# Kernel tuning notes

Hardware: AMD Instinct MI355X
Metric: run time of the kernel (lower is better)

## Reference

```python
import jax, jax.numpy as jnp
import numpy as np

NUM_HEADS = 8

def setup_inputs() -> dict:
    key = jax.random.key(0)
    k1, k2, k3 = jax.random.split(key, 3)
    B, N, C = 4, 4096, 512
    x = jax.random.normal(k1, (B, N, C), dtype=jnp.float32)
    w_qkv = jax.random.normal(k2, (C, 3 * C), dtype=jnp.float32) * (1.0 / np.sqrt(C))
    w_proj = jax.random.normal(k3, (C, C), dtype=jnp.float32) * (1.0 / np.sqrt(C))
    b_proj = jnp.zeros((C,), dtype=jnp.float32)
    return {"x": x, "w_qkv": w_qkv, "w_proj": w_proj, "b_proj": b_proj}

def reference(x, w_qkv, w_proj, b_proj):
    B, N, C = x.shape
    H = NUM_HEADS
    D = C // H
    # qkv projection (no bias), split into q, k, v of shape [B, H, N, D]
    qkv = (x @ w_qkv).reshape(B, N, 3, H, D)
    qkv = jnp.transpose(qkv, (2, 0, 3, 1, 4))
    q, k, v = qkv[0], qkv[1], qkv[2]
    # q: softmax over head_dim; k: elu(k)+1 then softmax over sequence dim
    q = jax.nn.softmax(q, axis=-1)
    k = jax.nn.softmax(jax.nn.elu(k) + 1.0, axis=-2)
    # linear attention: context = k^T @ v  -> [B, H, D, D]
    context = jnp.einsum('bhnd,bhne->bhde', k, v)
    # out = q @ context -> [B, H, N, D]
    out = jnp.einsum('bhnd,bhde->bhne', q, context)
    out = jnp.transpose(out, (0, 2, 1, 3)).reshape(B, N, C)
    # output projection (dropout with p=0.0 is identity)
    return out @ w_proj + b_proj
```

## Files before the change

### kernel.cpp

```cpp
#include <hip/hip_runtime.h>
#include <hip/hip_bf16.h>

typedef unsigned short u16;
typedef __attribute__((ext_vector_type(8))) short bhalf8;
typedef __attribute__((ext_vector_type(4))) float fx4;

struct __align__(8) US4 { u16 v[4]; };

__device__ __forceinline__ u16 f2bf(float x) {
  union { float f; unsigned int u; } c; c.f = x;
  unsigned int r = c.u + 0x7FFFu + ((c.u >> 16) & 1u);
  return (u16)(r >> 16);
}

__device__ __forceinline__ float bf2f(u16 v) {
  union { unsigned int u; float f; } c; c.u = ((unsigned int)v) << 16;
  return c.f;
}

__device__ __forceinline__ void gload16(const void* g, void* l) {
  __builtin_amdgcn_global_load_lds((const __attribute__((address_space(1))) void*)g,
                                   (__attribute__((address_space(3))) void*)l,
                                   16, 0, 0);
}

#define MFMA16(a, b, c) __builtin_amdgcn_mfma_f32_16x16x32_bf16((a), (b), (c), 0, 0, 0)

__global__ __launch_bounds__(256)
void k_prep(const float* __restrict__ x, u16* __restrict__ xb,
            const float* __restrict__ wqkv, u16* __restrict__ wqT,
            const float* __restrict__ wproj, u16* __restrict__ wpT) {
  __shared__ float tile[64][65];
  const int bx = blockIdx.x;
  const int t = threadIdx.x;
  if (bx < 8192) {
    int i = bx * 256 + t;
    float4 v = ((const float4*)x)[i];
    US4 o;
    o.v[0] = f2bf(v.x); o.v[1] = f2bf(v.y); o.v[2] = f2bf(v.z); o.v[3] = f2bf(v.w);
    ((US4*)xb)[i] = o;
    return;
  }
  const float* in; u16* out; int C, remap, bx2;
  if (bx < 8384) { in = wqkv; out = wqT; C = 1536; remap = 1; bx2 = bx - 8192; }
  else           { in = wproj; out = wpT; C = 512;  remap = 0; bx2 = bx - 8384; }
  const int rt = bx2 & 7, ct = bx2 >> 3;
  const int r0 = rt * 64, c0 = ct * 64;
  #pragma unroll
  for (int i = 0; i < 16; ++i) {
    int e = i * 256 + t;
    int rr = e >> 6, cc = e & 63;
    tile[rr][cc] = in[(r0 + rr) * C + c0 + cc];
  }
  __syncthreads();
  #pragma unroll
  for (int i = 0; i < 16; ++i) {
    int e = i * 256 + t;
    int rr = e >> 6, cc = e & 63;
    int orow = c0 + rr;
    if (remap && orow >= 512) {
      int region = (orow - 512) >> 9;
      int within = (orow - 512) & 511;
      int h = within >> 6;
      orow = 512 + h * 128 + region * 64 + (within & 63);
    }
    out[orow * 512 + r0 + cc] = f2bf(tile[cc][rr]);
  }
}

__device__ __forceinline__ void gemm_core512(const char* Ab, const char* Bb,
                                             char* As, char* Bs, fx4 acc[4][4]) {
  const int t = threadIdx.x;
  const int w = t >> 6, l = t & 63;
  const int wm = w >> 2, wn = w & 3;
  #pragma unroll 1
  for (int kt = 0; kt < 8; ++kt) {
    __syncthreads();
    const int kb = kt * 128;
    #pragma unroll
    for (int i = 0; i < 2; ++i) {
      int off = (i * 512 + t) * 16;
      int row = off >> 7;
      int scol = (off & 127) ^ ((row & 7) << 4);
      gload16(Ab + row * 1024 + kb + scol, As + off);
    }
    #pragma unroll
    for (int i = 0; i < 4; ++i) {
      int off = (i * 512 + t) * 16;
      int row = off >> 7;
      int scol = (off & 127) ^ ((row & 7) << 4);
      gload16(Bb + row * 1024 + kb + scol, Bs + off);
    }
    asm volatile("s_waitcnt vmcnt(0)" ::: "memory");
    __syncthreads();
    #pragma unroll
    for (int ks = 0; ks < 2; ++ks) {
      bhalf8 af[4], bfv[4];
      const int kbyte = ks * 64 + ((l >> 4) * 16);
      #pragma unroll
      for (int f = 0; f < 4; ++f) {
        int ra = wm * 64 + f * 16 + (l & 15);
        af[f] = *(const bhalf8*)(As + ra * 128 + (kbyte ^ ((ra & 7) << 4)));
        int rb = wn * 64 + f * 16 + (l & 15);
        bfv[f] = *(const bhalf8*)(Bs + rb * 128 + (kbyte ^ ((rb & 7) << 4)));
      }
      #pragma unroll
      for (int fm = 0; fm < 4; ++fm)
        #pragma unroll
        for (int fn = 0; fn < 4; ++fn)
          acc[fm][fn] = MFMA16(af[fm], bfv[fn], acc[fm][fn]);
    }
  }
}

__device__ __forceinline__ void gemm_core256(const char* Ab, const char* Bb,
                                             char* As, char* Bs, fx4 acc[4][4]) {
  const int t = threadIdx.x;
  const int w = t >> 6, l = t & 63;
  const int wm = w >> 1, wn = w & 1;
  #pragma unroll 1
  for (int kt = 0; kt < 8; ++kt) {
    __syncthreads();
    const int kb = kt * 128;
    #pragma unroll
    for (int j = 0; j < 4; ++j) {
      int off = ((j * 4 + w) * 64 + l) * 16;
      int row = off >> 7;
      int scol = (off & 127) ^ ((row & 7) << 4);
      gload16(Ab + row * 1024 + kb + scol, As + off);
      gload16(Bb + row * 1024 + kb + scol, Bs + off);
    }
    asm volatile("s_waitcnt vmcnt(0)" ::: "memory");
    __syncthreads();
    #pragma unroll
    for (int ks = 0; ks < 2; ++ks) {
      bhalf8 af[4], bfv[4];
      const int kbyte = ks * 64 + ((l >> 4) * 16);
      #pragma unroll
      for (int f = 0; f < 4; ++f) {
        int ra = wm * 64 + f * 16 + (l & 15);
        af[f] = *(const bhalf8*)(As + ra * 128 + (kbyte ^ ((ra & 7) << 4)));
        int rb = wn * 64 + f * 16 + (l & 15);
        bfv[f] = *(const bhalf8*)(Bs + rb * 128 + (kbyte ^ ((rb & 7) << 4)));
      }
      #pragma unroll
      for (int fm = 0; fm < 4; ++fm)
        #pragma unroll
        for (int fn = 0; fn < 4; ++fn)
          acc[fm][fn] = MFMA16(af[fm], bfv[fn], acc[fm][fn]);
    }
  }
}

__global__ __launch_bounds__(512, 4)
void k_qkv_gemm(const char* __restrict__ xb, const char* __restrict__ wqT,
                u16* __restrict__ qhat, u16* __restrict__ ctx_part,
                float* __restrict__ z_part) {
  __shared__ __align__(16) char lds[65536];
  const int bx = blockIdx.x;
  const int tM = bx & 127, tN = bx >> 7;
  fx4 acc[4][4];
  const fx4 z4 = {0.f, 0.f, 0.f, 0.f};
  #pragma unroll
  for (int i = 0; i < 4; ++i)
    #pragma unroll
    for (int j = 0; j < 4; ++j) acc[i][j] = z4;

  gemm_core512(xb + tM * 131072, wqT + tN * 262144, lds, lds + 16384, acc);

  const int t = threadIdx.x, w = t >> 6, l = t & 63;
  const int wm = w >> 2, wn = w & 3;
  const int m0 = tM * 128 + wm * 64;
  const int c0 = tN * 256 + wn * 64;

  if (tN < 2) {
    #pragma unroll
    for (int fm = 0; fm < 4; ++fm) {
      #pragma unroll
      for (int fn = 0; fn < 4; ++fn)
        #pragma unroll
        for (int r = 0; r < 4; ++r)
          acc[fm][fn][r] = __expf(acc[fm][fn][r]);
      fx4 s = acc[fm][0] + acc[fm][1] + acc[fm][2] + acc[fm][3];
      fx4 inv;
      #pragma unroll
      for (int r = 0; r < 4; ++r) {
        float sv = s[r];
        sv += __shfl_xor(sv, 1, 64);
        sv += __shfl_xor(sv, 2, 64);
        sv += __shfl_xor(sv, 4, 64);
        sv += __shfl_xor(sv, 8, 64);
        inv[r] = 1.0f / sv;
      }
      #pragma unroll
      for (int fn = 0; fn < 4; ++fn)
        #pragma unroll
        for (int r = 0; r < 4; ++r) {
          int m = m0 + fm * 16 + ((l >> 4) * 4) + r;
          int c = c0 + fn * 16 + (l & 15);
          qhat[m * 512 + c] = f2bf(acc[fm][fn][r] * inv[r]);
        }
    }
  } else {
    const int hpair = tN - 2;
    const int b = tM >> 5;
    const int mt = tM & 31;
    const int hl = wn >> 1;
    const bool isK = ((wn & 1) == 0);
    char* ktb = lds + hl * 32768;
    char* vtb = ktb + 16384;
    char* dstb = isK ? ktb : vtb;
    __syncthreads();
    #pragma unroll
    for (int fm = 0; fm < 4; ++fm)
      #pragma unroll
      for (int fn = 0; fn < 4; ++fn) {
        int d = fn * 16 + (l & 15);
        int n0 = wm * 64 + fm * 16 + ((l >> 4) * 4);
        US4 p;
        #pragma unroll
        for (int r = 0; r < 4; ++r) {
          float v = acc[fm][fn][r];
          if (isK) { float tt = v > 0.f ? v + 1.f : __expf(v); v = __expf(tt); }
          p.v[r] = f2bf(v);
        }
        *(US4*)(dstb + d * 256 + ((2 * n0) ^ ((d & 7) << 4))) = p;
      }
    __syncthreads();
    const int hl2 = w >> 2;
    const int bh = b * 8 + hpair * 2 + hl2;
    char* kb2 = lds + hl2 * 32768;
    char* vb2 = kb2 + 16384;
    const int d0 = (w & 3) * 16;
    fx4 cacc[4]; fx4 zacc = z4;
    #pragma unroll
    for (int fe = 0; fe < 4; ++fe) cacc[fe] = z4;
    bhalf8 ones;
    #pragma unroll
    for (int i = 0; i < 8; ++i) ones[i] = (short)0x3F80;
    #pragma unroll
    for (int kk = 0; kk < 4; ++kk) {
      int nbyte = kk * 64 + ((l >> 4) * 16);
      int d = d0 + (l & 15);
      bhalf8 a = *(const bhalf8*)(kb2 + d * 256 + (nbyte ^ ((d & 7) << 4)));
      #pragma unroll
      for (int fe = 0; fe < 4; ++fe) {
        int e = fe * 16 + (l & 15);
        bhalf8 bv = *(const bhalf8*)(vb2 + e * 256 + (nbyte ^ ((e & 7) << 4)));
        cacc[fe] = MFMA16(a, bv, cacc[fe]);
      }
      zacc = MFMA16(a, ones, zacc);
    }
    u16* cp = ctx_part + (bh * 32 + mt) * 4096;
    #pragma unroll
    for (int fe = 0; fe < 4; ++fe)
      #pragma unroll
      for (int r = 0; r < 4; ++r) {
        int d = d0 + ((l >> 4) * 4) + r;
        int e = fe * 16 + (l & 15);
        cp[d * 64 + e] = f2bf(cacc[fe][r]);
      }
    if ((l & 15) == 0) {
      #pragma unroll
      for (int r = 0; r < 4; ++r)
        z_part[(bh * 32 + mt) * 64 + d0 + ((l >> 4) * 4) + r] = zacc[r];
    }
  }
}

__global__ __launch_bounds__(256)
void k_reduce(const u16* __restrict__ ctx_part, float* __restrict__ ctx32) {
  const int bid = blockIdx.x;
  const int bh = bid >> 2;
  const int idx0 = (bid & 3) * 1024 + threadIdx.x * 4;
  float s0 = 0.f, s1 = 0.f, s2 = 0.f, s3 = 0.f;
  #pragma unroll
  for (int mt = 0; mt < 32; ++mt) {
    US4 p = *(const US4*)(ctx_part + (bh * 32 + mt) * 4096 + idx0);
    s0 += bf2f(p.v[0]); s1 += bf2f(p.v[1]); s2 += bf2f(p.v[2]); s3 += bf2f(p.v[3]);
  }
  float4 o; o.x = s0; o.y = s1; o.z = s2; o.w = s3;
  *(float4*)(ctx32 + bh * 4096 + idx0) = o;
}

__global__ __launch_bounds__(256, 1)
void k_w2(const float* __restrict__ ctx32, const float* __restrict__ z_part,
          const u16* __restrict__ wpT, u16* __restrict__ W2T) {
  const int bh = blockIdx.x;
  const int b = bh >> 3, h = bh & 7;
  __shared__ float zinv[64];
  __shared__ __align__(16) u16 alds[64][72];
  const int t = threadIdx.x;
  if (t < 64) {
    float zs = 0.f;
    #pragma unroll
    for (int mt = 0; mt < 32; ++mt) zs += z_part[(bh * 32 + mt) * 64 + t];
    zinv[t] = 1.0f / zs;
  }
  __syncthreads();
  #pragma unroll
  for (int i = 0; i < 16; ++i) {
    int idx = i * 256 + t;
    int d = idx >> 6, e = idx & 63;
    alds[d][e] = f2bf(ctx32[bh * 4096 + idx] * zinv[d]);
  }
  __syncthreads();
  const int w = t >> 6, l = t & 63;
  fx4 acc[4][8];
  const fx4 z4 = {0.f, 0.f, 0.f, 0.f};
  #pragma unroll
  for (int i = 0; i < 4; ++i)
    #pragma unroll
    for (int j = 0; j < 8; ++j) acc[i][j] = z4;
  #pragma unroll
  for (int ks = 0; ks < 2; ++ks) {
    bhalf8 af[4];
    #pragma unroll
    for (int fm = 0; fm < 4; ++fm) {
      int row = fm * 16 + (l & 15);
      af[fm] = *(const bhalf8*)((const char*)alds + row * 144 + ks * 64 + ((l >> 4) * 16));
    }
    #pragma unroll
    for (int fn = 0; fn < 8; ++fn) {
      int c = w * 128 + fn * 16 + (l & 15);
      bhalf8 bv = *(const bhalf8*)(wpT + c * 512 + h * 64 + ks * 32 + ((l >> 4) * 8));
      #pragma unroll
      for (int fm = 0; fm < 4; ++fm)
        acc[fm][fn] = MFMA16(af[fm], bv, acc[fm][fn]);
    }
  }
  #pragma unroll
  for (int fm = 0; fm < 4; ++fm)
    #pragma unroll
    for (int fn = 0; fn < 8; ++fn) {
      int c = w * 128 + fn * 16 + (l & 15);
      int d0 = fm * 16 + ((l >> 4) * 4);
      US4 p;
      #pragma unroll
      for (int r = 0; r < 4; ++r) p.v[r] = f2bf(acc[fm][fn][r]);
      *(US4*)(W2T + (b * 512 + c) * 512 + h * 64 + d0) = p;
    }
}

__global__ __launch_bounds__(256, 2)
void k_out_gemm(const char* __restrict__ qhat, const char* __restrict__ W2T,
                const float* __restrict__ bproj, float* __restrict__ outp) {
  __shared__ __align__(16) char lds[32768];
  const int bx = blockIdx.x;
  const int tM = bx & 127, tN = bx >> 7;
  const int b = tM >> 5;
  fx4 acc[4][4];
  const fx4 z4 = {0.f, 0.f, 0.f, 0.f};
  #pragma unroll
  for (int i = 0; i < 4; ++i)
    #pragma unroll
    for (int j = 0; j < 4; ++j) acc[i][j] = z4;

  gemm_core256(qhat + tM * 131072, W2T + b * 524288 + tN * 131072, lds, lds + 16384, acc);

  const int t = threadIdx.x, w = t >> 6, l = t & 63;
  const int wm = w >> 1, wn = w & 1;
  const int m0 = tM * 128 + wm * 64;
  const int c0 = tN * 128 + wn * 64;
  #pragma unroll
  for (int fm = 0; fm < 4; ++fm)
    #pragma unroll
    for (int fn = 0; fn < 4; ++fn) {
      int c = c0 + fn * 16 + (l & 15);
      float bp = bproj[c];
      #pragma unroll
      for (int r = 0; r < 4; ++r) {
        int m = m0 + fm * 16 + ((l >> 4) * 4) + r;
        outp[m * 512 + c] = acc[fm][fn][r] + bp;
      }
    }
}

extern "C" void kernel_launch(void* const* d_in, const int* in_sizes, int n_in,
                              void* d_out, int out_size, void* d_ws, size_t ws_size,
                              hipStream_t stream) {
  (void)in_sizes; (void)n_in; (void)out_size;
  const float* x     = (const float*)d_in[0];
  const float* wqkv  = (const float*)d_in[1];
  const float* wproj = (const float*)d_in[2];
  const float* bproj = (const float*)d_in[3];
  float* outp = (float*)d_out;
  char* ws = (char*)d_ws;

  char* xb   = ws;
  char* wqT  = ws + 16777216;
  char* wpT  = ws + 18350080;
  char* qhat = ws + 18874368;
  char* ctxp = ws + 35651584;
  char* zp   = ws + 44040192;
  char* ctx32= ws + 44302336;
  char* w2t  = ws + 44826624;
  if (ws_size < 46923776) return;

  k_prep<<<8448, 256, 0, stream>>>(x, (u16*)xb, wqkv, (u16*)wqT, wproj, (u16*)wpT);
  k_qkv_gemm<<<768, 512, 0, stream>>>(xb, wqT, (u16*)qhat, (u16*)ctxp, (float*)zp);
  k_reduce<<<128, 256, 0, stream>>>((const u16*)ctxp, (float*)ctx32);
  k_w2<<<32, 256, 0, stream>>>((const float*)ctx32, (const float*)zp, (const u16*)wpT, (u16*)w2t);
  k_out_gemm<<<512, 256, 0, stream>>>(qhat, w2t, bproj, outp);
}
```

Measured before the change: 80.43 us.

## Enlarge QKV GEMM tile to 256x256 with double-buffered ping-pong LDS pipeline

The QKV GEMM tile grows from 128x256 to 256x256, halving the grid to 384 blocks. The main loop now double-buffers LDS (128 KB), stages the next k-tile in quarters between MFMA quadrants, and uses s_setprio and split barriers to overlap global loads with matrix math. The partial context and normaliser counts drop from 32 to 16 per head, which shrinks the reduce work and the workspace. In exchange, more registers and LDS are used per block, which lowers occupancy, and the tail wave is coarser with fewer blocks.

```diff
diff --git a/kernel.cpp b/kernel.cpp
--- a/kernel.cpp
+++ b/kernel.cpp
@@ -68,120 +68,146 @@
   }
 }
 
-__device__ __forceinline__ void gemm_core512(const char* Ab, const char* Bb,
-                                             char* As, char* Bs, fx4 acc[4][4]) {
-  const int t = threadIdx.x;
-  const int w = t >> 6, l = t & 63;
-  const int wm = w >> 2, wn = w & 3;
-  #pragma unroll 1
-  for (int kt = 0; kt < 8; ++kt) {
-    __syncthreads();
-    const int kb = kt * 128;
-    #pragma unroll
-    for (int i = 0; i < 2; ++i) {
-      int off = (i * 512 + t) * 16;
-      int row = off >> 7;
-      int scol = (off & 127) ^ ((row & 7) << 4);
-      gload16(Ab + row * 1024 + kb + scol, As + off);
-    }
-    #pragma unroll
-    for (int i = 0; i < 4; ++i) {
-      int off = (i * 512 + t) * 16;
-      int row = off >> 7;
-      int scol = (off & 127) ^ ((row & 7) << 4);
-      gload16(Bb + row * 1024 + kb + scol, Bs + off);
-    }
-    asm volatile("s_waitcnt vmcnt(0)" ::: "memory");
-    __syncthreads();
-    #pragma unroll
-    for (int ks = 0; ks < 2; ++ks) {
-      bhalf8 af[4], bfv[4];
-      const int kbyte = ks * 64 + ((l >> 4) * 16);
-      #pragma unroll
-      for (int f = 0; f < 4; ++f) {
-        int ra = wm * 64 + f * 16 + (l & 15);
-        af[f] = *(const bhalf8*)(As + ra * 128 + (kbyte ^ ((ra & 7) << 4)));
-        int rb = wn * 64 + f * 16 + (l & 15);
-        bfv[f] = *(const bhalf8*)(Bs + rb * 128 + (kbyte ^ ((rb & 7) << 4)));
-      }
-      #pragma unroll
-      for (int fm = 0; fm < 4; ++fm)
-        #pragma unroll
-        for (int fn = 0; fn < 4; ++fn)
-          acc[fm][fn] = MFMA16(af[fm], bfv[fn], acc[fm][fn]);
-    }
-  }
-}
-
-__device__ __forceinline__ void gemm_core256(const char* Ab, const char* Bb,
-                                             char* As, char* Bs, fx4 acc[4][4]) {
-  const int t = threadIdx.x;
-  const int w = t >> 6, l = t & 63;
-  const int wm = w >> 1, wn = w & 1;
-  #pragma unroll 1
-  for (int kt = 0; kt < 8; ++kt) {
-    __syncthreads();
-    const int kb = kt * 128;
-    #pragma unroll
-    for (int j = 0; j < 4; ++j) {
-      int off = ((j * 4 + w) * 64 + l) * 16;
-      int row = off >> 7;
-      int scol = (off & 127) ^ ((row & 7) << 4);
-      gload16(Ab + row * 1024 + kb + scol, As + off);
-      gload16(Bb + row * 1024 + kb + scol, Bs + off);
-    }
-    asm volatile("s_waitcnt vmcnt(0)" ::: "memory");
-    __syncthreads();
-    #pragma unroll
-    for (int ks = 0; ks < 2; ++ks) {
-      bhalf8 af[4], bfv[4];
-      const int kbyte = ks * 64 + ((l >> 4) * 16);
-      #pragma unroll
-      for (int f = 0; f < 4; ++f) {
-        int ra = wm * 64 + f * 16 + (l & 15);
-        af[f] = *(const bhalf8*)(As + ra * 128 + (kbyte ^ ((ra & 7) << 4)));
-        int rb = wn * 64 + f * 16 + (l & 15);
-        bfv[f] = *(const bhalf8*)(Bs + rb * 128 + (kbyte ^ ((rb & 7) << 4)));
-      }
-      #pragma unroll
-      for (int fm = 0; fm < 4; ++fm)
-        #pragma unroll
-        for (int fn = 0; fn < 4; ++fn)
-          acc[fm][fn] = MFMA16(af[fm], bfv[fn], acc[fm][fn]);
-    }
-  }
-}
-
-__global__ __launch_bounds__(512, 4)
+__device__ __forceinline__ void stage_half_A(const char* Ab, char* buf, int kt, int hf, int t) {
+  #pragma unroll
+  for (int j = 0; j < 2; ++j) {
+    int o = (j * 512 + t) * 16;
+    int r = o >> 7;
+    int m = (r & 63) | ((r >> 6) << 7) | (hf << 6);
+    gload16(Ab + m * 1024 + kt * 128 + ((o & 127) ^ ((r & 7) << 4)),
+            buf + hf * 16384 + o);
+  }
+}
+__device__ __forceinline__ void stage_half_B(const char* Bb, char* buf, int kt, int hf, int t) {
+  #pragma unroll
+  for (int j = 0; j < 2; ++j) {
+    int o = (j * 512 + t) * 16;
+    int r = o >> 7;
+    int c = (r & 31) | ((r >> 5) << 6) | (hf << 5);
+    gload16(Bb + c * 1024 + kt * 128 + ((o & 127) ^ ((r & 7) << 4)),
+            buf + 32768 + hf * 16384 + o);
+  }
+}
+
+__global__ __launch_bounds__(512, 2)
 void k_qkv_gemm(const char* __restrict__ xb, const char* __restrict__ wqT,
                 u16* __restrict__ qhat, u16* __restrict__ ctx_part,
                 float* __restrict__ z_part) {
-  __shared__ __align__(16) char lds[65536];
+  __shared__ __align__(16) char lds[131072];
   const int bx = blockIdx.x;
-  const int tM = bx & 127, tN = bx >> 7;
-  fx4 acc[4][4];
+  const int tM = bx & 63, tN = bx >> 6;
+  const char* Ab = xb + tM * 262144;
+  const char* Bb = wqT + tN * 262144;
+  const int tid = threadIdx.x;
+  const int w = tid >> 6, l = tid & 63;
+  const int wm = w >> 2, wn = w & 3;
+
+  fx4 acc[8][4];
   const fx4 z4 = {0.f, 0.f, 0.f, 0.f};
   #pragma unroll
-  for (int i = 0; i < 4; ++i)
+  for (int i = 0; i < 8; ++i)
     #pragma unroll
     for (int j = 0; j < 4; ++j) acc[i][j] = z4;
 
-  gemm_core512(xb + tM * 131072, wqT + tN * 262144, lds, lds + 16384, acc);
-
-  const int t = threadIdx.x, w = t >> 6, l = t & 63;
-  const int wm = w >> 2, wn = w & 3;
-  const int m0 = tM * 128 + wm * 64;
-  const int c0 = tN * 256 + wn * 64;
+  bhalf8 a[8], b0[4], b1[4];
+
+#define LOAD_A(As, mq) do {                                              \
+    _Pragma("unroll") for (int ks = 0; ks < 2; ++ks) {                   \
+      const int kb_ = ks * 64 + ((l >> 4) * 16);                         \
+      _Pragma("unroll") for (int fm = 0; fm < 4; ++fm) {                 \
+        int ra_ = wm * 64 + fm * 16 + (l & 15);                          \
+        a[ks * 4 + fm] = *(const bhalf8*)((As) + (mq) * 16384 +          \
+                         ra_ * 128 + (kb_ ^ ((ra_ & 7) << 4)));          \
+      } } } while (0)
+#define LOAD_B(Bs, nq, br) do {                                          \
+    _Pragma("unroll") for (int ks = 0; ks < 2; ++ks) {                   \
+      const int kb_ = ks * 64 + ((l >> 4) * 16);                         \
+      _Pragma("unroll") for (int fn = 0; fn < 2; ++fn) {                 \
+        int rb_ = wn * 32 + fn * 16 + (l & 15);                          \
+        br[ks * 2 + fn] = *(const bhalf8*)((Bs) + 32768 + (nq) * 16384 + \
+                          rb_ * 128 + (kb_ ^ ((rb_ & 7) << 4)));         \
+      } } } while (0)
+#define MFMA_QUAD(mq, nq, br) do {                                       \
+    __builtin_amdgcn_s_setprio(1);                                       \
+    _Pragma("unroll") for (int ks = 0; ks < 2; ++ks)                     \
+      _Pragma("unroll") for (int fm = 0; fm < 4; ++fm)                   \
+        _Pragma("unroll") for (int fn = 0; fn < 2; ++fn)                 \
+          acc[(mq) * 4 + fm][(nq) * 2 + fn] =                            \
+            MFMA16(a[ks * 4 + fm], br[ks * 2 + fn],                      \
+                   acc[(mq) * 4 + fm][(nq) * 2 + fn]);                   \
+    __builtin_amdgcn_s_setprio(0);                                       \
+  } while (0)
+#define BARX()  do { __builtin_amdgcn_s_barrier();                       \
+    __builtin_amdgcn_sched_barrier(0); } while (0)
+#define LGKM0() do { asm volatile("s_waitcnt lgkmcnt(0)" ::: "memory");  \
+    __builtin_amdgcn_sched_barrier(0); } while (0)
+#define VM(N)   asm volatile("s_waitcnt vmcnt(" #N ")" ::: "memory")
+
+  stage_half_A(Ab, lds, 0, 0, tid);
+  stage_half_B(Bb, lds, 0, 0, tid);
+  stage_half_B(Bb, lds, 0, 1, tid);
+  stage_half_A(Ab, lds, 0, 1, tid);
+  VM(4);
+  BARX();
+
+  #pragma unroll 1
+  for (int kt = 0; kt < 7; ++kt) {
+    const char* As = lds + (kt & 1) * 65536;
+    char* nbuf = lds + ((kt + 1) & 1) * 65536;
+    LOAD_A(As, 0); LOAD_B(As, 0, b0);
+    stage_half_A(Ab, nbuf, kt + 1, 0, tid);
+    __builtin_amdgcn_s_barrier(); LGKM0();
+    MFMA_QUAD(0, 0, b0);
+    VM(4); BARX();
+    LOAD_B(As, 1, b1);
+    stage_half_B(Bb, nbuf, kt + 1, 0, tid);
+    __builtin_amdgcn_s_barrier(); LGKM0();
+    MFMA_QUAD(0, 1, b1);
+    VM(4); BARX();
+    LOAD_A(As, 1);
+    stage_half_B(Bb, nbuf, kt + 1, 1, tid);
+    __builtin_amdgcn_s_barrier(); LGKM0();
+    MFMA_QUAD(1, 1, b1);
+    BARX();
+    stage_half_A(Ab, nbuf, kt + 1, 1, tid);
+    __builtin_amdgcn_s_barrier();
+    MFMA_QUAD(1, 0, b0);
+    VM(4); BARX();
+  }
+  {
+    const char* As = lds + 65536;
+    LOAD_A(As, 0); LOAD_B(As, 0, b0);
+    __builtin_amdgcn_s_barrier(); LGKM0();
+    MFMA_QUAD(0, 0, b0);
+    VM(2); BARX();
+    LOAD_B(As, 1, b1);
+    __builtin_amdgcn_s_barrier(); LGKM0();
+    MFMA_QUAD(0, 1, b1);
+    VM(0); BARX();
+    LOAD_A(As, 1);
+    __builtin_amdgcn_s_barrier(); LGKM0();
+    MFMA_QUAD(1, 1, b1);
+    BARX();
+    MFMA_QUAD(1, 0, b0);
+  }
+#undef LOAD_A
+#undef LOAD_B
+#undef MFMA_QUAD
+#undef BARX
+#undef LGKM0
+#undef VM
 
   if (tN < 2) {
-    #pragma unroll
-    for (int fm = 0; fm < 4; ++fm) {
-      #pragma unroll
-      for (int fn = 0; fn < 4; ++fn)
+    const int m0 = tM * 256 + wm * 128;
+    const int c0 = tN * 256 + wn * 64;
+    #pragma unroll
+    for (int i = 0; i < 8; ++i) {
+      #pragma unroll
+      for (int j = 0; j < 4; ++j)
         #pragma unroll
         for (int r = 0; r < 4; ++r)
-          acc[fm][fn][r] = __expf(acc[fm][fn][r]);
-      fx4 s = acc[fm][0] + acc[fm][1] + acc[fm][2] + acc[fm][3];
+          acc[i][j][r] = __expf(acc[i][j][r]);
+      fx4 s = acc[i][0] + acc[i][1] + acc[i][2] + acc[i][3];
       fx4 inv;
       #pragma unroll
       for (int r = 0; r < 4; ++r) {
@@ -193,44 +219,43 @@
         inv[r] = 1.0f / sv;
       }
       #pragma unroll
-      for (int fn = 0; fn < 4; ++fn)
+      for (int j = 0; j < 4; ++j)
         #pragma unroll
         for (int r = 0; r < 4; ++r) {
-          int m = m0 + fm * 16 + ((l >> 4) * 4) + r;
-          int c = c0 + fn * 16 + (l & 15);
-          qhat[m * 512 + c] = f2bf(acc[fm][fn][r] * inv[r]);
+          int m = m0 + i * 16 + ((l >> 4) * 4) + r;
+          int c = c0 + j * 16 + (l & 15);
+          qhat[m * 512 + c] = f2bf(acc[i][j][r] * inv[r]);
         }
     }
   } else {
     const int hpair = tN - 2;
-    const int b = tM >> 5;
-    const int mt = tM & 31;
+    const int b = tM >> 4, mt = tM & 15;
     const int hl = wn >> 1;
     const bool isK = ((wn & 1) == 0);
-    char* ktb = lds + hl * 32768;
-    char* vtb = ktb + 16384;
-    char* dstb = isK ? ktb : vtb;
     __syncthreads();
-    #pragma unroll
-    for (int fm = 0; fm < 4; ++fm)
-      #pragma unroll
-      for (int fn = 0; fn < 4; ++fn) {
-        int d = fn * 16 + (l & 15);
-        int n0 = wm * 64 + fm * 16 + ((l >> 4) * 4);
+    char* kbuf = lds + hl * 65536;
+    char* vbuf = kbuf + 32768;
+    char* dstb = isK ? kbuf : vbuf;
+    #pragma unroll
+    for (int i = 0; i < 8; ++i)
+      #pragma unroll
+      for (int j = 0; j < 4; ++j) {
+        int d = j * 16 + (l & 15);
+        int n0 = wm * 128 + i * 16 + ((l >> 4) * 4);
         US4 p;
         #pragma unroll
         for (int r = 0; r < 4; ++r) {
-          float v = acc[fm][fn][r];
+          float v = acc[i][j][r];
           if (isK) { float tt = v > 0.f ? v + 1.f : __expf(v); v = __expf(tt); }
           p.v[r] = f2bf(v);
         }
-        *(US4*)(dstb + d * 256 + ((2 * n0) ^ ((d & 7) << 4))) = p;
+        *(US4*)(dstb + d * 512 + ((2 * n0) ^ ((d & 7) << 4))) = p;
       }
     __syncthreads();
     const int hl2 = w >> 2;
     const int bh = b * 8 + hpair * 2 + hl2;
-    char* kb2 = lds + hl2 * 32768;
-    char* vb2 = kb2 + 16384;
+    char* kb2 = lds + hl2 * 65536;
+    char* vb2 = kb2 + 32768;
     const int d0 = (w & 3) * 16;
     fx4 cacc[4]; fx4 zacc = z4;
     #pragma unroll
@@ -239,19 +264,19 @@
     #pragma unroll
     for (int i = 0; i < 8; ++i) ones[i] = (short)0x3F80;
     #pragma unroll
-    for (int kk = 0; kk < 4; ++kk) {
+    for (int kk = 0; kk < 8; ++kk) {
       int nbyte = kk * 64 + ((l >> 4) * 16);
       int d = d0 + (l & 15);
-      bhalf8 a = *(const bhalf8*)(kb2 + d * 256 + (nbyte ^ ((d & 7) << 4)));
+      bhalf8 av = *(const bhalf8*)(kb2 + d * 512 + (nbyte ^ ((d & 7) << 4)));
       #pragma unroll
       for (int fe = 0; fe < 4; ++fe) {
         int e = fe * 16 + (l & 15);
-        bhalf8 bv = *(const bhalf8*)(vb2 + e * 256 + (nbyte ^ ((e & 7) << 4)));
-        cacc[fe] = MFMA16(a, bv, cacc[fe]);
-      }
-      zacc = MFMA16(a, ones, zacc);
-    }
-    u16* cp = ctx_part + (bh * 32 + mt) * 4096;
+        bhalf8 bv = *(const bhalf8*)(vb2 + e * 512 + (nbyte ^ ((e & 7) << 4)));
+        cacc[fe] = MFMA16(av, bv, cacc[fe]);
+      }
+      zacc = MFMA16(av, ones, zacc);
+    }
+    u16* cp = ctx_part + (bh * 16 + mt) * 4096;
     #pragma unroll
     for (int fe = 0; fe < 4; ++fe)
       #pragma unroll
@@ -263,7 +288,7 @@
     if ((l & 15) == 0) {
       #pragma unroll
       for (int r = 0; r < 4; ++r)
-        z_part[(bh * 32 + mt) * 64 + d0 + ((l >> 4) * 4) + r] = zacc[r];
+        z_part[(bh * 16 + mt) * 64 + d0 + ((l >> 4) * 4) + r] = zacc[r];
     }
   }
 }
@@ -275,8 +300,8 @@
   const int idx0 = (bid & 3) * 1024 + threadIdx.x * 4;
   float s0 = 0.f, s1 = 0.f, s2 = 0.f, s3 = 0.f;
   #pragma unroll
-  for (int mt = 0; mt < 32; ++mt) {
-    US4 p = *(const US4*)(ctx_part + (bh * 32 + mt) * 4096 + idx0);
+  for (int mt = 0; mt < 16; ++mt) {
+    US4 p = *(const US4*)(ctx_part + (bh * 16 + mt) * 4096 + idx0);
     s0 += bf2f(p.v[0]); s1 += bf2f(p.v[1]); s2 += bf2f(p.v[2]); s3 += bf2f(p.v[3]);
   }
   float4 o; o.x = s0; o.y = s1; o.z = s2; o.w = s3;
@@ -294,7 +319,7 @@
   if (t < 64) {
     float zs = 0.f;
     #pragma unroll
-    for (int mt = 0; mt < 32; ++mt) zs += z_part[(bh * 32 + mt) * 64 + t];
+    for (int mt = 0; mt < 16; ++mt) zs += z_part[(bh * 16 + mt) * 64 + t];
     zinv[t] = 1.0f / zs;
   }
   __syncthreads();
@@ -340,6 +365,45 @@
       for (int r = 0; r < 4; ++r) p.v[r] = f2bf(acc[fm][fn][r]);
       *(US4*)(W2T + (b * 512 + c) * 512 + h * 64 + d0) = p;
     }
+}
+
+__device__ __forceinline__ void gemm_core(const char* Ab, const char* Bb,
+                                          char* As, char* Bs, fx4 acc[4][4]) {
+  const int t = threadIdx.x;
+  const int w = t >> 6, l = t & 63;
+  const int wm = w >> 1, wn = w & 1;
+  #pragma unroll 1
+  for (int kt = 0; kt < 8; ++kt) {
+    __syncthreads();
+    const int kb = kt * 128;
+    #pragma unroll
+    for (int j = 0; j < 4; ++j) {
+      int off = ((j * 4 + w) * 64 + l) * 16;
+      int row = off >> 7;
+      int scol = (off & 127) ^ ((row & 7) << 4);
+      gload16(Ab + row * 1024 + kb + scol, As + off);
+      gload16(Bb + row * 1024 + kb + scol, Bs + off);
+    }
+    asm volatile("s_waitcnt vmcnt(0)" ::: "memory");
+    __syncthreads();
+    #pragma unroll
+    for (int ks = 0; ks < 2; ++ks) {
+      bhalf8 af[4], bfv[4];
+      const int kbyte = ks * 64 + ((l >> 4) * 16);
+      #pragma unroll
+      for (int f = 0; f < 4; ++f) {
+        int ra = wm * 64 + f * 16 + (l & 15);
+        af[f] = *(const bhalf8*)(As + ra * 128 + (kbyte ^ ((ra & 7) << 4)));
+        int rb = wn * 64 + f * 16 + (l & 15);
+        bfv[f] = *(const bhalf8*)(Bs + rb * 128 + (kbyte ^ ((rb & 7) << 4)));
+      }
+      #pragma unroll
+      for (int fm = 0; fm < 4; ++fm)
+        #pragma unroll
+        for (int fn = 0; fn < 4; ++fn)
+          acc[fm][fn] = MFMA16(af[fm], bfv[fn], acc[fm][fn]);
+    }
+  }
 }
 
 __global__ __launch_bounds__(256, 2)
@@ -356,7 +420,7 @@
     #pragma unroll
     for (int j = 0; j < 4; ++j) acc[i][j] = z4;
 
-  gemm_core256(qhat + tM * 131072, W2T + b * 524288 + tN * 131072, lds, lds + 16384, acc);
+  gemm_core(qhat + tM * 131072, W2T + b * 524288 + tN * 131072, lds, lds + 16384, acc);
 
   const int t = threadIdx.x, w = t >> 6, l = t & 63;
   const int wm = w >> 1, wn = w & 1;
@@ -392,13 +456,13 @@
   char* wpT  = ws + 18350080;
   char* qhat = ws + 18874368;
   char* ctxp = ws + 35651584;
-  char* zp   = ws + 44040192;
-  char* ctx32= ws + 44302336;
-  char* w2t  = ws + 44826624;
-  if (ws_size < 46923776) return;
+  char* zp   = ws + 39845888;
+  char* ctx32= ws + 39976960;
+  char* w2t  = ws + 40501248;
+  if (ws_size < 42598400) return;
 
   k_prep<<<8448, 256, 0, stream>>>(x, (u16*)xb, wqkv, (u16*)wqT, wproj, (u16*)wpT);
-  k_qkv_gemm<<<768, 512, 0, stream>>>(xb, wqT, (u16*)qhat, (u16*)ctxp, (float*)zp);
+  k_qkv_gemm<<<384, 512, 0, stream>>>(xb, wqT, (u16*)qhat, (u16*)ctxp, (float*)zp);
   k_reduce<<<128, 256, 0, stream>>>((const u16*)ctxp, (float*)ctx32);
   k_w2<<<32, 256, 0, stream>>>((const float*)ctx32, (const float*)zp, (const u16*)wpT, (u16*)w2t);
   k_out_gemm<<<512, 256, 0, stream>>>(qhat, w2t, bproj, outp);
```

Measured after the change: 84.27 us. +4.8%, slower.
